# Performance work log

Hardware: AMD Instinct MI355X
Metric: run time of the kernel (lower is better)

The kernel has to match this reference:

```python
import jax, jax.numpy as jnp
import numpy as np

XINT_MAX = 0.125; SCALE_STD = 0.2; ROTATE_MAX = 1.0; ANISO_STD = 0.2; XFRAC_STD = 0.125
BRIGHT_STD = 0.2; CONTRAST_STD = 0.5; HUE_MAX = 1.0; SAT_STD = 1.0
NOISE_STD = 0.1; CUTOUT_SIZE = 0.5


def _eye4(B):
    return jnp.tile(jnp.eye(4, dtype=jnp.float32), (B, 1, 1))


def _scale3d(sx, sy, sz):
    B = sx.shape[0]
    sy = jnp.broadcast_to(sy, (B,)); sz = jnp.broadcast_to(sz, (B,))
    return _eye4(B).at[:, 0, 0].set(sx).at[:, 1, 1].set(sy).at[:, 2, 2].set(sz)


def _translate3d(tx, ty, tz):
    B = tx.shape[0]
    return _eye4(B).at[:, 0, 3].set(tx).at[:, 1, 3].set(ty).at[:, 2, 3].set(tz)


def _rotz(theta):
    # rotate3d([0,0,1], theta)
    c, s = jnp.cos(theta), jnp.sin(theta)
    B = theta.shape[0]
    return _eye4(B).at[:, 0, 0].set(c).at[:, 0, 1].set(-s).at[:, 1, 0].set(s).at[:, 1, 1].set(c)


def _rot_luma(theta):
    # rotate3d around v=(1,1,1)/sqrt(3) (Rodrigues), embedded in 4x4
    a = 1.0 / np.sqrt(3.0); a2 = 1.0 / 3.0
    c, s = jnp.cos(theta), jnp.sin(theta); cc = 1.0 - c
    B = theta.shape[0]
    d = a2 * cc + c; m = a2 * cc - a * s; p = a2 * cc + a * s
    M = _eye4(B)
    M = M.at[:, 0, 0].set(d).at[:, 0, 1].set(m).at[:, 0, 2].set(p)
    M = M.at[:, 1, 0].set(p).at[:, 1, 1].set(d).at[:, 1, 2].set(m)
    M = M.at[:, 2, 0].set(m).at[:, 2, 1].set(p).at[:, 2, 2].set(d)
    return M


def _warp3d(images, G_inv):
    # trilinear grid-sample with zero padding; coords are image-centered pixels
    B, C, D, H, W = images.shape
    gx = jnp.arange(W, dtype=jnp.float32) - (W - 1) / 2.0
    gy = jnp.arange(H, dtype=jnp.float32) - (H - 1) / 2.0
    gz = jnp.arange(D, dtype=jnp.float32) - (D - 1) / 2.0
    Z, Y, X = jnp.meshgrid(gz, gy, gx, indexing='ij')  # [D,H,W]
    homog = jnp.stack([X, Y, Z, jnp.ones_like(X)], axis=-1)  # [D,H,W,4] (x,y,z,1)
    src = jnp.einsum('bij,dhwj->bdhwi', G_inv[:, :3, :], homog)  # [B,D,H,W,3]
    sx = src[..., 0] + (W - 1) / 2.0
    sy = src[..., 1] + (H - 1) / 2.0
    sz = src[..., 2] + (D - 1) / 2.0
    x0f = jnp.floor(sx); y0f = jnp.floor(sy); z0f = jnp.floor(sz)
    wx = sx - x0f; wy = sy - y0f; wz = sz - z0f
    x0 = x0f.astype(jnp.int32); y0 = y0f.astype(jnp.int32); z0 = z0f.astype(jnp.int32)

    def gather(iz, iy, ix):
        valid = (ix >= 0) & (ix < W) & (iy >= 0) & (iy < H) & (iz >= 0) & (iz < D)
        ixc = jnp.clip(ix, 0, W - 1); iyc = jnp.clip(iy, 0, H - 1); izc = jnp.clip(iz, 0, D - 1)
        vals = jax.vmap(lambda im, zz, yy, xx: im[:, zz, yy, xx])(images, izc, iyc, ixc)
        return vals * valid[:, None].astype(images.dtype)  # [B,C,D,H,W]

    out = jnp.zeros_like(images)
    for dz in (0, 1):
        for dy in (0, 1):
            for dx in (0, 1):
                w = ((wz if dz else 1 - wz) * (wy if dy else 1 - wy) * (wx if dx else 1 - wx))
                out = out + gather(z0 + dz, y0 + dy, x0 + dx) * w[:, None]
    return out


def setup_inputs() -> dict:
    key = jax.random.key(0)
    images = jax.random.normal(key, (16, 3, 64, 64, 64), dtype=jnp.float32)
    return {"images": images}


def reference(images):
    B, C, D, H, W = images.shape
    ks = list(jax.random.split(jax.random.key(42), 24)); ki = iter(ks)
    rand = lambda shape: jax.random.uniform(next(ki), shape, dtype=jnp.float32)
    randn = lambda shape: jax.random.normal(next(ki), shape, dtype=jnp.float32)
    ones = jnp.ones((B,), jnp.float32)

    # ---- geometric: compose inverse transform matrix (p=1 -> all gates pass) ----
    G = _eye4(B)
    i = jnp.floor(rand((B,)) * 2)                       # xflip
    G = G @ _scale3d(1 - 2 * i, ones, ones)
    i = jnp.floor(rand((B,)) * 4)                       # rotate90 about z
    G = G @ _rotz(-np.pi / 2 * i)
    t = (rand((B, 3)) * 2 - 1) * XINT_MAX               # integer translation
    G = G @ _translate3d(-jnp.round(t[:, 0] * W), -jnp.round(t[:, 1] * H), -jnp.round(t[:, 2] * D))
    s = jnp.exp2(randn((B,)) * SCALE_STD)               # isotropic scale (inv)
    G = G @ _scale3d(1 / s, 1 / s, 1 / s)
    theta = (rand((B,)) * 2 - 1) * np.pi * ROTATE_MAX   # pre-rotation
    G = G @ _rotz(-theta)
    s = jnp.exp2(randn((B,)) * ANISO_STD)               # anisotropic scale (inv)
    G = G @ _scale3d(1 / s, s, ones)
    theta = (rand((B,)) * 2 - 1) * np.pi * ROTATE_MAX   # post-rotation
    G = G @ _rotz(-theta)
    t = randn((B, 3)) * XFRAC_STD                       # fractional translation
    G = G @ _translate3d(-t[:, 0] * W, -t[:, 1] * H, -t[:, 2] * D)
    images = _warp3d(images, G)

    # ---- color: compose 4x4 homogeneous color matrix ----
    Cm = _eye4(B)
    b = randn((B,)) * BRIGHT_STD                        # brightness
    Cm = _translate3d(b, b, b) @ Cm
    c = jnp.exp2(randn((B,)) * CONTRAST_STD)            # contrast
    Cm = _scale3d(c, c, c) @ Cm
    v = jnp.asarray([1, 1, 1, 0], jnp.float32) / np.sqrt(3.0)
    vv = jnp.outer(v, v)
    i = jnp.floor(rand((B,)) * 2)                       # lumaflip
    Cm = (jnp.eye(4, dtype=jnp.float32) - 2 * vv * i[:, None, None]) @ Cm
    theta = (rand((B,)) * 2 - 1) * np.pi * HUE_MAX      # hue rotation about luma axis
    Cm = _rot_luma(theta) @ Cm
    s = jnp.exp2(randn((B,)) * SAT_STD)                 # saturation
    Cm = (vv + (jnp.eye(4, dtype=jnp.float32) - vv) * s[:, None, None]) @ Cm
    images = (jnp.einsum('bij,bjdhw->bidhw', Cm[:, :3, :3], images)
              + Cm[:, :3, 3][:, :, None, None, None])

    # ---- noise ----
    sigma = jnp.abs(randn((B,))) * NOISE_STD
    images = images + randn(images.shape) * sigma[:, None, None, None, None]

    # ---- cutout (3D box) ----
    center = rand((B, 3))
    half = CUTOUT_SIZE / 2
    fx = (jnp.arange(W, dtype=jnp.float32) + 0.5) / W
    fy = (jnp.arange(H, dtype=jnp.float32) + 0.5) / H
    fz = (jnp.arange(D, dtype=jnp.float32) + 0.5) / D
    mx = jnp.abs(fx[None, :] - center[:, 0:1]) >= half  # [B,W]
    my = jnp.abs(fy[None, :] - center[:, 1:2]) >= half  # [B,H]
    mz = jnp.abs(fz[None, :] - center[:, 2:3]) >= half  # [B,D]
    mask = (mx[:, None, None, None, :] | my[:, None, None, :, None] | mz[:, None, :, None, None])
    return images * mask.astype(images.dtype)
```

## Files before the change

kernel.cpp:

```cpp
#include <hip/hip_runtime.h>
#include <cstring>
#include <cstdint>
#include <cmath>

__host__ __device__ static inline uint32_t rotl32(uint32_t v, int r) {
    return __builtin_rotateleft32(v, (unsigned)r);
}

__host__ __device__ static inline void tf2x32(uint32_t k0, uint32_t k1,
                                              uint32_t& x0, uint32_t& x1) {
    uint32_t ks2 = k0 ^ k1 ^ 0x1BD11BDAu;
    x0 += k0; x1 += k1;
#define TFR(r) { x0 += x1; x1 = rotl32(x1, r); x1 ^= x0; }
    TFR(13) TFR(15) TFR(26) TFR(6)
    x0 += k1;  x1 += ks2 + 1u;
    TFR(17) TFR(29) TFR(16) TFR(24)
    x0 += ks2; x1 += k0 + 2u;
    TFR(13) TFR(15) TFR(26) TFR(6)
    x0 += k0;  x1 += k1 + 3u;
    TFR(17) TFR(29) TFR(16) TFR(24)
    x0 += k1;  x1 += ks2 + 4u;
    TFR(13) TFR(15) TFR(26) TFR(6)
    x0 += ks2; x1 += k0 + 5u;
#undef TFR
}

__host__ __device__ static inline uint32_t pbits(uint32_t k0, uint32_t k1, uint32_t i) {
    uint32_t a = 0u, b = i;
    tf2x32(k0, k1, a, b);
    return a ^ b;
}

__host__ __device__ static inline float bits_to_u01(uint32_t bits) {
    uint32_t u = (bits >> 9) | 0x3f800000u;
    float f; memcpy(&f, &u, 4);
    return f - 1.0f;
}

__host__ static inline float erfinv_f(float x) {
    float w = -log1pf(-x * x);
    float p;
    if (w < 5.0f) {
        w = w - 2.5f;
        p = 2.81022636e-08f;
        p = fmaf(p, w, 3.43273939e-07f);
        p = fmaf(p, w, -3.5233877e-06f);
        p = fmaf(p, w, -4.39150654e-06f);
        p = fmaf(p, w, 0.00021858087f);
        p = fmaf(p, w, -0.00125372503f);
        p = fmaf(p, w, -0.00417768164f);
        p = fmaf(p, w, 0.246640727f);
        p = fmaf(p, w, 1.50140941f);
    } else {
        w = sqrtf(w) - 3.0f;
        p = -0.000200214257f;
        p = fmaf(p, w, 0.000100950558f);
        p = fmaf(p, w, 0.00134934322f);
        p = fmaf(p, w, -0.00367342844f);
        p = fmaf(p, w, 0.00573950773f);
        p = fmaf(p, w, -0.0076224613f);
        p = fmaf(p, w, 0.00943887047f);
        p = fmaf(p, w, 1.00167406f);
        p = fmaf(p, w, 2.83297682f);
    }
    return p * x;
}

__host__ static inline float normal_from_bits(uint32_t bits) {
    const float LO = -0.999999940395355224609375f;
    float u01 = bits_to_u01(bits);
    float u = u01 * 2.0f + LO;
    u = (u > LO) ? u : LO;
    return 1.4142135623730951f * erfinv_f(u);
}

__device__ __forceinline__ float normal_fast(uint32_t bits) {
    const float LO = -0.999999940395355224609375f;
    uint32_t u = (bits >> 9) | 0x3f800000u;
    float x = fmaf(__uint_as_float(u) - 1.0f, 2.0f, LO);
    x = fmaxf(x, LO);
    float t = fmaf(x, -x, 1.0f);
    float lg = __log2f(t);
    float p;
    if (__builtin_expect(lg > -7.2134752044448170f, 1)) {
        float w = fmaf(lg, -0.6931471805599453f, -2.5f);
        p = 2.81022636e-08f;
        p = fmaf(p, w, 3.43273939e-07f);
        p = fmaf(p, w, -3.5233877e-06f);
        p = fmaf(p, w, -4.39150654e-06f);
        p = fmaf(p, w, 0.00021858087f);
        p = fmaf(p, w, -0.00125372503f);
        p = fmaf(p, w, -0.00417768164f);
        p = fmaf(p, w, 0.246640727f);
        p = fmaf(p, w, 1.50140941f);
    } else {
        float w = sqrtf(lg * -0.6931471805599453f) - 3.0f;
        p = -0.000200214257f;
        p = fmaf(p, w, 0.000100950558f);
        p = fmaf(p, w, 0.00134934322f);
        p = fmaf(p, w, -0.00367342844f);
        p = fmaf(p, w, 0.00573950773f);
        p = fmaf(p, w, -0.0076224613f);
        p = fmaf(p, w, 0.00943887047f);
        p = fmaf(p, w, 1.00167406f);
        p = fmaf(p, w, 2.83297682f);
    }
    return 1.4142135623730951f * p * x;
}

__device__ __forceinline__ void noise3(uint32_t k0, uint32_t k1, uint32_t l,
                                       float& n0, float& n1, float& n2) {
    const uint32_t ks2 = k0 ^ k1 ^ 0x1BD11BDAu;
    uint32_t a0 = k0, b0 = l + k1;
    uint32_t a1 = k0, b1 = (l + 262144u) + k1;
    uint32_t a2 = k0, b2 = (l + 524288u) + k1;
#define R3(r)      { a0 += b0; b0 = rotl32(b0, r); b0 ^= a0; \
                     a1 += b1; b1 = rotl32(b1, r); b1 ^= a1; \
                     a2 += b2; b2 = rotl32(b2, r); b2 ^= a2; }
#define INJ(ka,kb) { a0 += (ka); b0 += (kb); a1 += (ka); b1 += (kb); a2 += (ka); b2 += (kb); }
    R3(13) R3(15) R3(26) R3(6)  INJ(k1,  ks2 + 1u)
    R3(17) R3(29) R3(16) R3(24) INJ(ks2, k0  + 2u)
    R3(13) R3(15) R3(26) R3(6)  INJ(k0,  k1  + 3u)
    R3(17) R3(29) R3(16) R3(24) INJ(k1,  ks2 + 4u)
    R3(13) R3(15) R3(26) R3(6)  INJ(ks2, k0  + 5u)
#undef R3
#undef INJ
    n0 = normal_fast(a0 ^ b0);
    n1 = normal_fast(a1 ^ b1);
    n2 = normal_fast(a2 ^ b2);
}

struct M4 { float m[4][4]; };

static M4 m4_eye() {
    M4 r;
    for (int i = 0; i < 4; ++i)
        for (int j = 0; j < 4; ++j) r.m[i][j] = (i == j) ? 1.0f : 0.0f;
    return r;
}
static M4 m4_mul(const M4& A, const M4& B) {
    M4 r;
    for (int i = 0; i < 4; ++i)
        for (int j = 0; j < 4; ++j) {
            float s = 0.0f;
            for (int k = 0; k < 4; ++k) s += A.m[i][k] * B.m[k][j];
            r.m[i][j] = s;
        }
    return r;
}
static M4 m4_scale(float sx, float sy, float sz) {
    M4 r = m4_eye(); r.m[0][0] = sx; r.m[1][1] = sy; r.m[2][2] = sz; return r;
}
static M4 m4_trans(float tx, float ty, float tz) {
    M4 r = m4_eye(); r.m[0][3] = tx; r.m[1][3] = ty; r.m[2][3] = tz; return r;
}
static M4 m4_rotz(float th) {
    float c = cosf(th), s = sinf(th);
    M4 r = m4_eye();
    r.m[0][0] = c; r.m[0][1] = -s; r.m[1][0] = s; r.m[1][1] = c;
    return r;
}
static M4 m4_rotluma(float th) {
    const float a  = 0.57735026918962576f;
    const float a2 = 1.0f / 3.0f;
    float c = cosf(th), s = sinf(th), cc = 1.0f - c;
    float d  = a2 * cc + c;
    float mm = a2 * cc - a * s;
    float pp = a2 * cc + a * s;
    M4 r = m4_eye();
    r.m[0][0] = d;  r.m[0][1] = mm; r.m[0][2] = pp;
    r.m[1][0] = pp; r.m[1][1] = d;  r.m[1][2] = mm;
    r.m[2][0] = mm; r.m[2][1] = pp; r.m[2][2] = d;
    return r;
}

struct AugParams {
    float G[16][12];
    float C[16][12];
    float sigma[16];
    float cx[16], cy[16], cz[16];
    uint32_t nk0, nk1;
};

static void build_params(AugParams& P) {
    uint32_t sk0[24], sk1[24];
    for (int j = 0; j < 24; ++j) {
        uint32_t a = 0u, b = (uint32_t)j;
        tf2x32(0u, 42u, a, b);
        sk0[j] = a; sk1[j] = b;
    }

    float u_xf[16], u_r90[16], u_ti[48], n_sc[16], u_r1[16], n_an[16], u_r2[16];
    float n_tf[48], n_br[16], n_ct[16], u_lf[16], u_hue[16], n_sat[16], n_sig[16], u_cut[48];

    auto fill_u = [&](int j, int n, float* o) {
        for (int i = 0; i < n; ++i) o[i] = bits_to_u01(pbits(sk0[j], sk1[j], (uint32_t)i));
    };
    auto fill_n = [&](int j, int n, float* o) {
        for (int i = 0; i < n; ++i) o[i] = normal_from_bits(pbits(sk0[j], sk1[j], (uint32_t)i));
    };

    fill_u(0, 16, u_xf);  fill_u(1, 16, u_r90);  fill_u(2, 48, u_ti);
    fill_n(3, 16, n_sc);  fill_u(4, 16, u_r1);   fill_n(5, 16, n_an);
    fill_u(6, 16, u_r2);  fill_n(7, 48, n_tf);   fill_n(8, 16, n_br);
    fill_n(9, 16, n_ct);  fill_u(10, 16, u_lf);  fill_u(11, 16, u_hue);
    fill_n(12, 16, n_sat); fill_n(13, 16, n_sig); fill_u(15, 48, u_cut);
    P.nk0 = sk0[14]; P.nk1 = sk1[14];

    const float PI_F = 3.14159265358979323846f;
    const float HPI_F = 1.5707963267948966f;

    for (int b = 0; b < 16; ++b) {
        M4 G = m4_eye();
        float i1 = floorf(u_xf[b] * 2.0f);
        G = m4_mul(G, m4_scale(1.0f - 2.0f * i1, 1.0f, 1.0f));
        float i2 = floorf(u_r90[b] * 4.0f);
        G = m4_mul(G, m4_rotz(-HPI_F * i2));
        float t0 = (u_ti[3 * b + 0] * 2.0f - 1.0f) * 0.125f;
        float t1 = (u_ti[3 * b + 1] * 2.0f - 1.0f) * 0.125f;
        float t2 = (u_ti[3 * b + 2] * 2.0f - 1.0f) * 0.125f;
        G = m4_mul(G, m4_trans(-rintf(t0 * 64.0f), -rintf(t1 * 64.0f), -rintf(t2 * 64.0f)));
        float s = exp2f(n_sc[b] * 0.2f);
        G = m4_mul(G, m4_scale(1.0f / s, 1.0f / s, 1.0f / s));
        float th1 = (u_r1[b] * 2.0f - 1.0f) * PI_F;
        G = m4_mul(G, m4_rotz(-th1));
        float s2 = exp2f(n_an[b] * 0.2f);
        G = m4_mul(G, m4_scale(1.0f / s2, s2, 1.0f));
        float th2 = (u_r2[b] * 2.0f - 1.0f) * PI_F;
        G = m4_mul(G, m4_rotz(-th2));
        float f0 = n_tf[3 * b + 0] * 0.125f;
        float f1 = n_tf[3 * b + 1] * 0.125f;
        float f2 = n_tf[3 * b + 2] * 0.125f;
        G = m4_mul(G, m4_trans(-f0 * 64.0f, -f1 * 64.0f, -f2 * 64.0f));

        M4 C = m4_eye();
        float br = n_br[b] * 0.2f;
        C = m4_mul(m4_trans(br, br, br), C);
        float ct = exp2f(n_ct[b] * 0.5f);
        C = m4_mul(m4_scale(ct, ct, ct), C);
        const float va = 0.57735026918962576f;
        float v4[4] = { va, va, va, 0.0f };
        float ilf = floorf(u_lf[b] * 2.0f);
        M4 L;
        for (int r = 0; r < 4; ++r)
            for (int c = 0; c < 4; ++c)
                L.m[r][c] = ((r == c) ? 1.0f : 0.0f) - 2.0f * (v4[r] * v4[c]) * ilf;
        C = m4_mul(L, C);
        float thh = (u_hue[b] * 2.0f - 1.0f) * PI_F;
        C = m4_mul(m4_rotluma(thh), C);
        float ss = exp2f(n_sat[b] * 1.0f);
        M4 S;
        for (int r = 0; r < 4; ++r)
            for (int c = 0; c < 4; ++c) {
                float vv = v4[r] * v4[c];
                S.m[r][c] = vv + (((r == c) ? 1.0f : 0.0f) - vv) * ss;
            }
        C = m4_mul(S, C);

        P.sigma[b] = fabsf(n_sig[b]) * 0.1f;
        P.cx[b] = u_cut[3 * b + 0];
        P.cy[b] = u_cut[3 * b + 1];
        P.cz[b] = u_cut[3 * b + 2];
        for (int r = 0; r < 3; ++r)
            for (int c = 0; c < 4; ++c) {
                P.G[b][r * 4 + c] = G.m[r][c];
                P.C[b][r * 4 + c] = C.m[r][c];
            }
    }
}

__global__ __launch_bounds__(256) void repack_kernel(const float* __restrict__ in,
                                                     float4* __restrict__ ws4) {
    const int t = blockIdx.x * 256 + threadIdx.x;
    const int b = t >> 18;
    const int vox = t & 262143;
    const float* p = in + (size_t)b * 786432 + vox;
    float4 q;
    q.x = p[0];
    q.y = p[262144];
    q.z = p[524288];
    q.w = 0.0f;
    ws4[t] = q;
}

__global__ __launch_bounds__(256, 4) void aug_kernel4(const float4* __restrict__ ws4,
                                                      float* __restrict__ out,
                                                      AugParams P) {
    const int bid = blockIdx.x;
    const int b = bid >> 10;
    const int vox = ((bid & 1023) << 8) | threadIdx.x;
    const int x = vox & 63;
    const int y = (vox >> 6) & 63;
    const int z = vox >> 12;

    const float* Gb = P.G[b];
    const float hx = (float)x - 31.5f;
    const float hy = (float)y - 31.5f;
    const float hz = (float)z - 31.5f;
    float sx = Gb[0] * hx + Gb[1] * hy + Gb[2]  * hz + Gb[3]  + 31.5f;
    float sy = Gb[4] * hx + Gb[5] * hy + Gb[6]  * hz + Gb[7]  + 31.5f;
    float sz = Gb[8] * hx + Gb[9] * hy + Gb[10] * hz + Gb[11] + 31.5f;

    float fx = floorf(sx), fy = floorf(sy), fz = floorf(sz);
    float wx = sx - fx, wy = sy - fy, wz = sz - fz;
    int ix = (int)fx, iy = (int)fy, iz = (int)fz;

    float xw0 = ((unsigned)ix       < 64u) ? 1.0f - wx : 0.0f;
    float xw1 = ((unsigned)(ix + 1) < 64u) ? wx        : 0.0f;
    float yw0 = ((unsigned)iy       < 64u) ? 1.0f - wy : 0.0f;
    float yw1 = ((unsigned)(iy + 1) < 64u) ? wy        : 0.0f;
    float zw0 = ((unsigned)iz       < 64u) ? 1.0f - wz : 0.0f;
    float zw1 = ((unsigned)(iz + 1) < 64u) ? wz        : 0.0f;

    int xc0 = min(max(ix, 0), 63),       xc1 = min(max(ix + 1, 0), 63);
    int yo0 = min(max(iy, 0), 63) << 6,  yo1 = min(max(iy + 1, 0), 63) << 6;
    int zo0 = min(max(iz, 0), 63) << 12, zo1 = min(max(iz + 1, 0), 63) << 12;

    float w00 = zw0 * yw0, w01 = zw0 * yw1, w10 = zw1 * yw0, w11 = zw1 * yw1;
    int   o00 = zo0 + yo0, o01 = zo0 + yo1, o10 = zo1 + yo0, o11 = zo1 + yo1;

    const float4* __restrict__ w4 = ws4 + (size_t)b * 262144;
    float r = 0.0f, g = 0.0f, bl = 0.0f;
#define CORNER4(W, O) { \
    float4 qa = w4[(O) + xc0]; float4 qb = w4[(O) + xc1]; \
    const float wg0 = (W) * xw0, wg1 = (W) * xw1; \
    r  = fmaf(qa.x, wg0, r);  r  = fmaf(qb.x, wg1, r);  \
    g  = fmaf(qa.y, wg0, g);  g  = fmaf(qb.y, wg1, g);  \
    bl = fmaf(qa.z, wg0, bl); bl = fmaf(qb.z, wg1, bl); }
    CORNER4(w00, o00) CORNER4(w01, o01) CORNER4(w10, o10) CORNER4(w11, o11)
#undef CORNER4

    const uint32_t l0 = (uint32_t)b * 786432u + (uint32_t)vox;
    float n0, n1, n2;
    noise3(P.nk0, P.nk1, l0, n0, n1, n2);

    const float* Cb = P.C[b];
    const float sg = P.sigma[b];
    float o0 = fmaf(Cb[0], r, fmaf(Cb[1], g, fmaf(Cb[2],  bl, Cb[3])));
    float o1 = fmaf(Cb[4], r, fmaf(Cb[5], g, fmaf(Cb[6],  bl, Cb[7])));
    float o2 = fmaf(Cb[8], r, fmaf(Cb[9], g, fmaf(Cb[10], bl, Cb[11])));
    o0 = fmaf(n0, sg, o0);
    o1 = fmaf(n1, sg, o1);
    o2 = fmaf(n2, sg, o2);

    float fxn = ((float)x + 0.5f) * 0.015625f;
    float fyn = ((float)y + 0.5f) * 0.015625f;
    float fzn = ((float)z + 0.5f) * 0.015625f;
    bool keep = (fabsf(fxn - P.cx[b]) >= 0.25f) ||
                (fabsf(fyn - P.cy[b]) >= 0.25f) ||
                (fabsf(fzn - P.cz[b]) >= 0.25f);
    float mk = keep ? 1.0f : 0.0f;

    size_t ob = (size_t)b * 786432 + (size_t)vox;
    out[ob]           = o0 * mk;
    out[ob + 262144]  = o1 * mk;
    out[ob + 524288]  = o2 * mk;
}

__global__ __launch_bounds__(256, 4) void aug_kernel_planar(const float* __restrict__ in,
                                                            float* __restrict__ out,
                                                            AugParams P) {
    const int bid = blockIdx.x;
    const int b = bid >> 10;
    const int vox = ((bid & 1023) << 8) | threadIdx.x;
    const int x = vox & 63;
    const int y = (vox >> 6) & 63;
    const int z = vox >> 12;

    const float* Gb = P.G[b];
    const float hx = (float)x - 31.5f;
    const float hy = (float)y - 31.5f;
    const float hz = (float)z - 31.5f;
    float sx = Gb[0] * hx + Gb[1] * hy + Gb[2]  * hz + Gb[3]  + 31.5f;
    float sy = Gb[4] * hx + Gb[5] * hy + Gb[6]  * hz + Gb[7]  + 31.5f;
    float sz = Gb[8] * hx + Gb[9] * hy + Gb[10] * hz + Gb[11] + 31.5f;

    float fx = floorf(sx), fy = floorf(sy), fz = floorf(sz);
    float wx = sx - fx, wy = sy - fy, wz = sz - fz;
    int ix = (int)fx, iy = (int)fy, iz = (int)fz;

    float xw0 = ((unsigned)ix       < 64u) ? 1.0f - wx : 0.0f;
    float xw1 = ((unsigned)(ix + 1) < 64u) ? wx        : 0.0f;
    float yw0 = ((unsigned)iy       < 64u) ? 1.0f - wy : 0.0f;
    float yw1 = ((unsigned)(iy + 1) < 64u) ? wy        : 0.0f;
    float zw0 = ((unsigned)iz       < 64u) ? 1.0f - wz : 0.0f;
    float zw1 = ((unsigned)(iz + 1) < 64u) ? wz        : 0.0f;

    int xc0 = min(max(ix, 0), 63),       xc1 = min(max(ix + 1, 0), 63);
    int yo0 = min(max(iy, 0), 63) << 6,  yo1 = min(max(iy + 1, 0), 63) << 6;
    int zo0 = min(max(iz, 0), 63) << 12, zo1 = min(max(iz + 1, 0), 63) << 12;

    float w00 = zw0 * yw0, w01 = zw0 * yw1, w10 = zw1 * yw0, w11 = zw1 * yw1;
    int   o00 = zo0 + yo0, o01 = zo0 + yo1, o10 = zo1 + yo0, o11 = zo1 + yo1;

    const float* __restrict__ imb = in + (size_t)b * 786432;
    float r = 0.0f, g = 0.0f, bl = 0.0f;
#define CORNER(W, O) { \
    const int off0 = (O) + xc0, off1 = (O) + xc1; \
    const float wg0 = (W) * xw0, wg1 = (W) * xw1; \
    r  = fmaf(imb[off0],          wg0, r);  r  = fmaf(imb[off1],          wg1, r);  \
    g  = fmaf(imb[262144 + off0], wg0, g);  g  = fmaf(imb[262144 + off1], wg1, g);  \
    bl = fmaf(imb[524288 + off0], wg0, bl); bl = fmaf(imb[524288 + off1], wg1, bl); }
    CORNER(w00, o00) CORNER(w01, o01) CORNER(w10, o10) CORNER(w11, o11)
#undef CORNER

    const uint32_t l0 = (uint32_t)b * 786432u + (uint32_t)vox;
    float n0, n1, n2;
    noise3(P.nk0, P.nk1, l0, n0, n1, n2);

    const float* Cb = P.C[b];
    const float sg = P.sigma[b];
    float o0 = fmaf(Cb[0], r, fmaf(Cb[1], g, fmaf(Cb[2],  bl, Cb[3])));
    float o1 = fmaf(Cb[4], r, fmaf(Cb[5], g, fmaf(Cb[6],  bl, Cb[7])));
    float o2 = fmaf(Cb[8], r, fmaf(Cb[9], g, fmaf(Cb[10], bl, Cb[11])));
    o0 = fmaf(n0, sg, o0);
    o1 = fmaf(n1, sg, o1);
    o2 = fmaf(n2, sg, o2);

    float fxn = ((float)x + 0.5f) * 0.015625f;
    float fyn = ((float)y + 0.5f) * 0.015625f;
    float fzn = ((float)z + 0.5f) * 0.015625f;
    bool keep = (fabsf(fxn - P.cx[b]) >= 0.25f) ||
                (fabsf(fyn - P.cy[b]) >= 0.25f) ||
                (fabsf(fzn - P.cz[b]) >= 0.25f);
    float mk = keep ? 1.0f : 0.0f;

    size_t ob = (size_t)b * 786432 + (size_t)vox;
    out[ob]           = o0 * mk;
    out[ob + 262144]  = o1 * mk;
    out[ob + 524288]  = o2 * mk;
}

extern "C" void kernel_launch(void* const* d_in, const int* in_sizes, int n_in,
                              void* d_out, int out_size, void* d_ws, size_t ws_size,
                              hipStream_t stream) {
    const float* in = (const float*)d_in[0];
    float* out = (float*)d_out;

    AugParams P;
    build_params(P);

    const size_t need = (size_t)16 * 262144 * sizeof(float4);
    if (ws_size >= need) {
        float4* ws4 = (float4*)d_ws;
        repack_kernel<<<dim3(16384), dim3(256), 0, stream>>>(in, ws4);
        aug_kernel4<<<dim3(16384), dim3(256), 0, stream>>>(ws4, out, P);
    } else {
        aug_kernel_planar<<<dim3(16384), dim3(256), 0, stream>>>(in, out, P);
    }
}
```

Measured before the change: 63.45 us.

## Move noise generation into repack kernel and store it as packed fp16

Generates the per-voxel Gaussian noise inside the memory-bound repack pass and stores it as packed half precision in the workspace. The augment kernel then reads the noise instead of running Threefry itself, which is meant to hide the RNG arithmetic behind the repack's memory traffic. The cost is extra workspace writes and reads, plus reduced noise precision from fp16 round-toward-zero conversion.

```diff
diff --git a/kernel.cpp b/kernel.cpp
--- a/kernel.cpp
+++ b/kernel.cpp
@@ -2,6 +2,8 @@
 #include <cstring>
 #include <cstdint>
 #include <cmath>
+
+typedef __fp16 half2v __attribute__((ext_vector_type(2)));
 
 __host__ __device__ static inline uint32_t rotl32(uint32_t v, int r) {
     return __builtin_rotateleft32(v, (unsigned)r);
@@ -269,6 +271,111 @@
     }
 }
 
+__global__ __launch_bounds__(256) void repack_noise_kernel(const float* __restrict__ in,
+                                                           float4* __restrict__ ws4,
+                                                           uint2* __restrict__ nz,
+                                                           uint32_t nk0, uint32_t nk1) {
+    const int t = blockIdx.x * 256 + threadIdx.x;
+    const int b = t >> 18;
+    const int vox = t & 262143;
+    const float* p = in + (size_t)b * 786432 + vox;
+    float4 q;
+    q.x = p[0];
+    q.y = p[262144];
+    q.z = p[524288];
+    q.w = 0.0f;
+
+    const uint32_t l0 = (uint32_t)b * 786432u + (uint32_t)vox;
+    float n0, n1, n2;
+    noise3(nk0, nk1, l0, n0, n1, n2);
+    half2v p01 = __builtin_amdgcn_cvt_pkrtz(n0, n1);
+    half2v p2x = __builtin_amdgcn_cvt_pkrtz(n2, 0.0f);
+    uint2 nv;
+    memcpy(&nv.x, &p01, 4);
+    memcpy(&nv.y, &p2x, 4);
+
+    ws4[t] = q;
+    nz[t] = nv;
+}
+
+__global__ __launch_bounds__(256, 4) void aug_kernel4n(const float4* __restrict__ ws4,
+                                                       const uint2* __restrict__ nz,
+                                                       float* __restrict__ out,
+                                                       AugParams P) {
+    const int bid = blockIdx.x;
+    const int b = bid >> 10;
+    const int vox = ((bid & 1023) << 8) | threadIdx.x;
+    const int x = vox & 63;
+    const int y = (vox >> 6) & 63;
+    const int z = vox >> 12;
+
+    const float* Gb = P.G[b];
+    const float hx = (float)x - 31.5f;
+    const float hy = (float)y - 31.5f;
+    const float hz = (float)z - 31.5f;
+    float sx = Gb[0] * hx + Gb[1] * hy + Gb[2]  * hz + Gb[3]  + 31.5f;
+    float sy = Gb[4] * hx + Gb[5] * hy + Gb[6]  * hz + Gb[7]  + 31.5f;
+    float sz = Gb[8] * hx + Gb[9] * hy + Gb[10] * hz + Gb[11] + 31.5f;
+
+    float fx = floorf(sx), fy = floorf(sy), fz = floorf(sz);
+    float wx = sx - fx, wy = sy - fy, wz = sz - fz;
+    int ix = (int)fx, iy = (int)fy, iz = (int)fz;
+
+    float xw0 = ((unsigned)ix       < 64u) ? 1.0f - wx : 0.0f;
+    float xw1 = ((unsigned)(ix + 1) < 64u) ? wx        : 0.0f;
+    float yw0 = ((unsigned)iy       < 64u) ? 1.0f - wy : 0.0f;
+    float yw1 = ((unsigned)(iy + 1) < 64u) ? wy        : 0.0f;
+    float zw0 = ((unsigned)iz       < 64u) ? 1.0f - wz : 0.0f;
+    float zw1 = ((unsigned)(iz + 1) < 64u) ? wz        : 0.0f;
+
+    int xc0 = min(max(ix, 0), 63),       xc1 = min(max(ix + 1, 0), 63);
+    int yo0 = min(max(iy, 0), 63) << 6,  yo1 = min(max(iy + 1, 0), 63) << 6;
+    int zo0 = min(max(iz, 0), 63) << 12, zo1 = min(max(iz + 1, 0), 63) << 12;
+
+    float w00 = zw0 * yw0, w01 = zw0 * yw1, w10 = zw1 * yw0, w11 = zw1 * yw1;
+    int   o00 = zo0 + yo0, o01 = zo0 + yo1, o10 = zo1 + yo0, o11 = zo1 + yo1;
+
+    const float4* __restrict__ w4 = ws4 + (size_t)b * 262144;
+    uint2 nv = nz[(size_t)b * 262144 + vox];
+
+    float r = 0.0f, g = 0.0f, bl = 0.0f;
+#define CORNER4(W, O) { \
+    float4 qa = w4[(O) + xc0]; float4 qb = w4[(O) + xc1]; \
+    const float wg0 = (W) * xw0, wg1 = (W) * xw1; \
+    r  = fmaf(qa.x, wg0, r);  r  = fmaf(qb.x, wg1, r);  \
+    g  = fmaf(qa.y, wg0, g);  g  = fmaf(qb.y, wg1, g);  \
+    bl = fmaf(qa.z, wg0, bl); bl = fmaf(qb.z, wg1, bl); }
+    CORNER4(w00, o00) CORNER4(w01, o01) CORNER4(w10, o10) CORNER4(w11, o11)
+#undef CORNER4
+
+    half2v p01, p2x;
+    memcpy(&p01, &nv.x, 4);
+    memcpy(&p2x, &nv.y, 4);
+    float n0 = (float)p01.x, n1 = (float)p01.y, n2 = (float)p2x.x;
+
+    const float* Cb = P.C[b];
+    const float sg = P.sigma[b];
+    float o0 = fmaf(Cb[0], r, fmaf(Cb[1], g, fmaf(Cb[2],  bl, Cb[3])));
+    float o1 = fmaf(Cb[4], r, fmaf(Cb[5], g, fmaf(Cb[6],  bl, Cb[7])));
+    float o2 = fmaf(Cb[8], r, fmaf(Cb[9], g, fmaf(Cb[10], bl, Cb[11])));
+    o0 = fmaf(n0, sg, o0);
+    o1 = fmaf(n1, sg, o1);
+    o2 = fmaf(n2, sg, o2);
+
+    float fxn = ((float)x + 0.5f) * 0.015625f;
+    float fyn = ((float)y + 0.5f) * 0.015625f;
+    float fzn = ((float)z + 0.5f) * 0.015625f;
+    bool keep = (fabsf(fxn - P.cx[b]) >= 0.25f) ||
+                (fabsf(fyn - P.cy[b]) >= 0.25f) ||
+                (fabsf(fzn - P.cz[b]) >= 0.25f);
+    float mk = keep ? 1.0f : 0.0f;
+
+    size_t ob = (size_t)b * 786432 + (size_t)vox;
+    out[ob]           = o0 * mk;
+    out[ob + 262144]  = o1 * mk;
+    out[ob + 524288]  = o2 * mk;
+}
+
 __global__ __launch_bounds__(256) void repack_kernel(const float* __restrict__ in,
                                                      float4* __restrict__ ws4) {
     const int t = blockIdx.x * 256 + threadIdx.x;
@@ -440,8 +547,15 @@
     AugParams P;
     build_params(P);
 
-    const size_t need = (size_t)16 * 262144 * sizeof(float4);
-    if (ws_size >= need) {
+    const size_t N = (size_t)16 * 262144;
+    const size_t need_rgba  = N * sizeof(float4);
+    const size_t need_noise = N * sizeof(uint2);
+    if (ws_size >= need_rgba + need_noise) {
+        float4* ws4 = (float4*)d_ws;
+        uint2*  nzb = (uint2*)((char*)d_ws + need_rgba);
+        repack_noise_kernel<<<dim3(16384), dim3(256), 0, stream>>>(in, ws4, nzb, P.nk0, P.nk1);
+        aug_kernel4n<<<dim3(16384), dim3(256), 0, stream>>>(ws4, nzb, out, P);
+    } else if (ws_size >= need_rgba) {
         float4* ws4 = (float4*)d_ws;
         repack_kernel<<<dim3(16384), dim3(256), 0, stream>>>(in, ws4);
         aug_kernel4<<<dim3(16384), dim3(256), 0, stream>>>(ws4, out, P);
```

Result: slower. 69.57 us (+9.6%).
